# Kernel tuning notes

Measured on AMD Instinct MI355X. Metric: run time of the kernel, lower is better.

Reference implementation:

```python
import itertools
import jax, jax.numpy as jnp
import numpy as np

# static block configuration
B, C, H, W, DIM, HEADS = 2, 4, 60, 120, 512, 8
WS = (2, 6, 12)          # window size (Wc, Wh, Ww)
SS = (1, 3, 6)           # shift size
N = WS[0] * WS[1] * WS[2]            # 144 tokens per window
C1, H1, W1 = C // WS[0], H // WS[1], W // WS[2]
NW = C1 * H1 * W1                    # windows per sample
DH = DIM // HEADS
EPS = 1e-6


def _attn_bias():
    """Static shifted-window attention bias (nW, N, N): 0 within group, -inf across.
    Mirrors compute_3d_shifted_window_mask (warped=True, longitude wrap merge)."""
    img = np.zeros((C, H, W), np.int32)
    c_sl = ((0, C - WS[0]), (C - WS[0], C - SS[0]), (C - SS[0], C))
    h_sl = ((0, H - WS[1]), (H - WS[1], H - SS[1]), (H - SS[1], H))
    w_sl = ((0, W - WS[2]), (W - WS[2], W - SS[2]), (W - SS[2], W))
    cnt = 0
    for (cs, ce), (hs, he), (ws_, we) in itertools.product(c_sl, h_sl, w_sl):
        img[cs:ce, hs:he, ws_:we] = cnt
        cnt += 1
    # warped (periodic longitude) group merges
    for i in range(3):
        for a, b in ((1, 2), (4, 5), (7, 8)):
            img[img == a + 9 * i] = b + 9 * i
    m = img.reshape(C1, WS[0], H1, WS[1], W1, WS[2])
    m = m.transpose(0, 2, 4, 1, 3, 5).reshape(NW, N)
    diff = m[:, None, :] - m[:, :, None]
    return jnp.asarray(np.where(diff != 0, -np.inf, 0.0).astype(np.float32))


_BIAS = _attn_bias()[None, :, None, :, :]  # (1, nW, 1, N, N)


def _ln(x, s, b):
    mu = x.mean(-1, keepdims=True)
    var = x.var(-1, keepdims=True)
    return (x - mu) / jnp.sqrt(var + EPS) * s + b


def setup_inputs() -> dict:
    key = jax.random.key(0)
    ks = jax.random.split(key, 6)
    s = 0.02
    return {
        "x": jax.random.normal(ks[0], (B, C * H * W, DIM), jnp.float32),
        "qkv_w": jax.random.normal(ks[1], (DIM, 3 * DIM), jnp.float32) * s,
        "qkv_b": jnp.zeros((3 * DIM,), jnp.float32),
        "proj_w": jax.random.normal(ks[2], (DIM, DIM), jnp.float32) * s,
        "proj_b": jnp.zeros((DIM,), jnp.float32),
        "norm1_scale": jnp.ones((DIM,), jnp.float32),
        "norm1_bias": jnp.zeros((DIM,), jnp.float32),
        "norm2_scale": jnp.ones((DIM,), jnp.float32),
        "norm2_bias": jnp.zeros((DIM,), jnp.float32),
        "mlp_w1": jax.random.normal(ks[3], (DIM, 4 * DIM), jnp.float32) * s,
        "mlp_b1": jnp.zeros((4 * DIM,), jnp.float32),
        "mlp_w2": jax.random.normal(ks[4], (4 * DIM, DIM), jnp.float32) * s,
        "mlp_b2": jnp.zeros((DIM,), jnp.float32),
    }


def reference(x, qkv_w, qkv_b, proj_w, proj_b, norm1_scale, norm1_bias,
              norm2_scale, norm2_bias, mlp_w1, mlp_b1, mlp_w2, mlp_b2):
    shortcut = x                                   # (B, L, D)
    h = _ln(x, norm1_scale, norm1_bias).reshape(B, C, H, W, DIM)
    # cyclic shift
    h = jnp.roll(h, (-SS[0], -SS[1], -SS[2]), axis=(1, 2, 3))
    # window partition: (B,C,H,W,D) -> (B*nW, N, D)
    h = h.reshape(B, C1, WS[0], H1, WS[1], W1, WS[2], DIM)
    h = h.transpose(0, 1, 3, 5, 2, 4, 6, 7).reshape(B * NW, N, DIM)
    # windowed multi-head self-attention
    qkv = h @ qkv_w + qkv_b                        # (B*nW, N, 3*D)
    qkv = qkv.reshape(B, NW, N, 3, HEADS, DH)
    q = qkv[..., 0, :, :].transpose(0, 1, 3, 2, 4)  # (B, nW, H, N, Dh)
    k = qkv[..., 1, :, :].transpose(0, 1, 3, 2, 4)
    v = qkv[..., 2, :, :].transpose(0, 1, 3, 2, 4)
    scale = 1.0 / float(np.sqrt(DH))
    attn = jnp.einsum("bwhnd,bwhmd->bwhnm", q, k) * scale + _BIAS
    attn = jax.nn.softmax(attn, axis=-1)
    o = jnp.einsum("bwhnm,bwhmd->bwhnd", attn, v)
    o = o.transpose(0, 1, 3, 2, 4).reshape(B * NW, N, DIM)
    o = o @ proj_w + proj_b
    # window reverse: (B*nW, N, D) -> (B,C,H,W,D)
    o = o.reshape(B, C1, H1, W1, WS[0], WS[1], WS[2], DIM)
    o = o.transpose(0, 1, 4, 2, 5, 3, 6, 7).reshape(B, C, H, W, DIM)
    # reverse cyclic shift
    o = jnp.roll(o, SS, axis=(1, 2, 3))
    x = shortcut + o.reshape(B, C * H * W, DIM)    # drop_path is identity
    # MLP block
    h2 = _ln(x, norm2_scale, norm2_bias)
    h2 = jax.nn.gelu(h2 @ mlp_w1 + mlp_b1) @ mlp_w2 + mlp_b2
    return x + h2
```

## Files before the change

kernel.cpp:

```cpp
#include <hip/hip_runtime.h>

typedef __attribute__((ext_vector_type(8))) short bf16x8;
typedef __attribute__((ext_vector_type(4))) float f32x4;
typedef __attribute__((ext_vector_type(8))) unsigned short u16x8;

#define BAR() __builtin_amdgcn_s_barrier()
#define VMC(n) asm volatile("s_waitcnt vmcnt(" #n ")" ::: "memory")
#define SB0() __builtin_amdgcn_sched_barrier(0)
#define WAITL(n) do { asm volatile("s_waitcnt lgkmcnt(" #n ")"); SB0(); } while (0)
#define DSRI(dst, base, imm) \
  asm volatile("ds_read_b128 %0, %1 offset:%2" : "=&v"(dst) : "v"(base), "i"(imm))

__device__ inline unsigned short f2bf(float f) {
  unsigned int u = __float_as_uint(f);
  u += 0x7fffu + ((u >> 16) & 1u);
  return (unsigned short)(u >> 16);
}

__device__ inline void gload_lds16(const void* g, void* l) {
  __builtin_amdgcn_global_load_lds(
      (const __attribute__((address_space(1))) void*)g,
      (__attribute__((address_space(3))) void*)l, 16, 0, 0);
}

__global__ void wtrans(const float* __restrict__ W, unsigned short* __restrict__ Wt,
                       int K, int N) {
  int idx = blockIdx.x * 256 + threadIdx.x;
  if (idx >= K * N) return;
  int k = idx / N, n = idx - k * N;
  Wt[(size_t)n * K + k] = f2bf(W[idx]);
}

template <int MODE>
__global__ void ln_k(const float* __restrict__ x, const float* __restrict__ sc,
                     const float* __restrict__ bi, unsigned short* __restrict__ o) {
  int t = blockIdx.x * 4 + (threadIdx.x >> 6);
  int l = threadIdx.x & 63;
  size_t src;
  if (MODE == 0) {
    int b = t / 28800, r = t - b * 28800;
    int win = r / 144, tok = r - win * 144;
    int c1 = win / 100, rem = win - c1 * 100;
    int h1 = rem / 10, w1 = rem - h1 * 10;
    int tc = tok / 72, tr = tok - tc * 72;
    int th = tr / 12, tw = tr - th * 12;
    int cs = c1 * 2 + tc, hs = h1 * 6 + th, wsp = w1 * 12 + tw;
    int co = (cs + 1) & 3;
    int ho = hs + 3; if (ho >= 60) ho -= 60;
    int wo = wsp + 6; if (wo >= 120) wo -= 120;
    src = ((size_t)b * 28800 + (co * 60 + ho) * 120 + wo) * 512;
  } else {
    src = (size_t)t * 512;
  }
  const float4* xr = (const float4*)(x + src);
  float4 v0 = xr[l * 2], v1 = xr[l * 2 + 1];
  float s = v0.x + v0.y + v0.z + v0.w + v1.x + v1.y + v1.z + v1.w;
  float s2 = v0.x * v0.x + v0.y * v0.y + v0.z * v0.z + v0.w * v0.w +
             v1.x * v1.x + v1.y * v1.y + v1.z * v1.z + v1.w * v1.w;
  #pragma unroll
  for (int o2 = 32; o2; o2 >>= 1) {
    s += __shfl_xor(s, o2);
    s2 += __shfl_xor(s2, o2);
  }
  float mean = s * (1.0f / 512.0f);
  float var = s2 * (1.0f / 512.0f) - mean * mean;
  float inv = rsqrtf(var + 1e-6f);
  const float4* scp = (const float4*)sc;
  const float4* bip = (const float4*)bi;
  float4 sa = scp[l * 2], sb = scp[l * 2 + 1];
  float4 ba = bip[l * 2], bb = bip[l * 2 + 1];
  u16x8 ov;
  ov[0] = f2bf((v0.x - mean) * inv * sa.x + ba.x);
  ov[1] = f2bf((v0.y - mean) * inv * sa.y + ba.y);
  ov[2] = f2bf((v0.z - mean) * inv * sa.z + ba.z);
  ov[3] = f2bf((v0.w - mean) * inv * sa.w + ba.w);
  ov[4] = f2bf((v1.x - mean) * inv * sb.x + bb.x);
  ov[5] = f2bf((v1.y - mean) * inv * sb.y + bb.y);
  ov[6] = f2bf((v1.z - mean) * inv * sb.z + bb.z);
  ov[7] = f2bf((v1.w - mean) * inv * sb.w + bb.w);
  *(u16x8*)&o[(size_t)t * 512 + l * 8] = ov;
}

template <int EPI>
__launch_bounds__(512, 2)
__global__ void gemm2p(const unsigned short* __restrict__ A,
                       const unsigned short* __restrict__ Bt,
                       const float* __restrict__ bias, void* __restrict__ outp,
                       const float* __restrict__ res, int M, int N, int K) {
  __shared__ __attribute__((aligned(16))) unsigned short ldsb[2][32768];
  const int tid = threadIdx.x;
  const int w = tid >> 6, l = tid & 63;
  const int wm = w >> 2, wn = w & 3;
  const int lane15 = l & 15;
  const int ntile = N >> 8;
  const int nwg = gridDim.x;
  const int q = nwg >> 3, r = nwg & 7;
  const int xcd = blockIdx.x & 7, idx8 = blockIdx.x >> 3;
  const int wgid = (xcd < r ? xcd * (q + 1) : r * (q + 1) + (xcd - r) * q) + idx8;
  const int bm = wgid / ntile, bn = wgid - bm * ntile;
  const int NT = K >> 6;

  int offA[4];
  {
    int rowt = tid >> 3, slot = tid & 7;
    int sl = slot ^ (rowt & 7);
    #pragma unroll
    for (int jj = 0; jj < 4; ++jj)
      offA[jj] = ((jj * 64 + rowt) * K + sl * 8) * 2;
  }
  const char* gA = (const char*)(A + (size_t)bm * 256 * K);
  const char* gB = (const char*)(Bt + (size_t)bn * 256 * K);

  unsigned lds0 = (unsigned)(unsigned long long)
      (__attribute__((address_space(3))) void*)(void*)&ldsb[0][0];
  const int rsw = (((l >> 4) ^ (lane15 & 7)) << 4);
  unsigned rA0 = lds0 + (unsigned)((wm * 128 + lane15) * 128 + rsw);
  unsigned rB0 = lds0 + 32768u + (unsigned)((wn * 64 + lane15) * 128 + rsw);
  unsigned rA1 = rA0 + 65536u, rB1 = rB0 + 65536u;
  unsigned short* pC = &ldsb[0][0];
  unsigned short* pN = &ldsb[1][0];

  f32x4 acc[8][4] = {};
  bf16x8 af[8], bf[4], ag[8], bg[4];

  auto STAGE = [&](unsigned short* pS) {
    #pragma unroll
    for (int jj = 0; jj < 4; ++jj)
      gload_lds16(gA + offA[jj], pS + jj * 4096 + tid * 8);
    #pragma unroll
    for (int jj = 0; jj < 4; ++jj)
      gload_lds16(gB + offA[jj], pS + 16384 + jj * 4096 + tid * 8);
    gA += 128;
    gB += 128;
  };

  STAGE(pC);
  VMC(0);
  BAR();

  for (int t = 0; t < NT; ++t) {
    if (t < NT - 1) STAGE(pN);
    DSRI(af[0], rA0, 0);    DSRI(af[1], rA0, 2048);
    DSRI(af[2], rA0, 4096); DSRI(af[3], rA0, 6144);
    DSRI(af[4], rA0, 8192); DSRI(af[5], rA0, 10240);
    DSRI(af[6], rA0, 12288); DSRI(af[7], rA0, 14336);
    DSRI(bf[0], rB0, 0);    DSRI(bf[1], rB0, 2048);
    DSRI(bf[2], rB0, 4096); DSRI(bf[3], rB0, 6144);
    {
      unsigned rAx = rA0 ^ 64u, rBx = rB0 ^ 64u;
      DSRI(ag[0], rAx, 0);    DSRI(ag[1], rAx, 2048);
      DSRI(ag[2], rAx, 4096); DSRI(ag[3], rAx, 6144);
      DSRI(ag[4], rAx, 8192); DSRI(ag[5], rAx, 10240);
      DSRI(ag[6], rAx, 12288); DSRI(ag[7], rAx, 14336);
      DSRI(bg[0], rBx, 0);    DSRI(bg[1], rBx, 2048);
      DSRI(bg[2], rBx, 4096); DSRI(bg[3], rBx, 6144);
    }
    WAITL(12);
    __builtin_amdgcn_s_setprio(1);
    #pragma unroll
    for (int mi = 0; mi < 8; ++mi)
      #pragma unroll
      for (int nf = 0; nf < 4; ++nf)
        acc[mi][nf] = __builtin_amdgcn_mfma_f32_16x16x32_bf16(
            af[mi], bf[nf], acc[mi][nf], 0, 0, 0);
    __builtin_amdgcn_s_setprio(0);
    WAITL(0);
    __builtin_amdgcn_s_setprio(1);
    #pragma unroll
    for (int mi = 0; mi < 8; ++mi)
      #pragma unroll
      for (int nf = 0; nf < 4; ++nf)
        acc[mi][nf] = __builtin_amdgcn_mfma_f32_16x16x32_bf16(
            ag[mi], bg[nf], acc[mi][nf], 0, 0, 0);
    __builtin_amdgcn_s_setprio(0);
    VMC(0);
    BAR();
    { unsigned tt = rA0; rA0 = rA1; rA1 = tt; }
    { unsigned tt = rB0; rB0 = rB1; rB1 = tt; }
    { unsigned short* tp = pC; pC = pN; pN = tp; }
  }

  float* outf = (float*)outp;
  unsigned short* outh = (unsigned short*)outp;
  #pragma unroll
  for (int mi = 0; mi < 8; ++mi) {
    #pragma unroll
    for (int j = 0; j < 4; ++j) {
      int grow = bm * 256 + wm * 128 + mi * 16 + ((l >> 4) << 2) + j;
      int win = 0, tok = 0;
      size_t rowbase = 0;
      if constexpr (EPI == 0) {
        win = grow / 144;
        tok = grow - win * 144;
      } else if constexpr (EPI == 1) {
        win = grow / 144;
        tok = grow - win * 144;
        int b = win / 200, wl = win - b * 200;
        int c1 = wl / 100, rem = wl - c1 * 100;
        int h1 = rem / 10, w1 = rem - h1 * 10;
        int tc = tok / 72, tr = tok - tc * 72;
        int th = tr / 12, tw = tr - th * 12;
        int cs = c1 * 2 + tc, hs = h1 * 6 + th, wsp = w1 * 12 + tw;
        int co = (cs + 1) & 3;
        int ho = hs + 3; if (ho >= 60) ho -= 60;
        int wo = wsp + 6; if (wo >= 120) wo -= 120;
        rowbase = ((size_t)b * 28800 + (co * 60 + ho) * 120 + wo) * 512;
      }
      #pragma unroll
      for (int nf = 0; nf < 4; ++nf) {
        int gcol = bn * 256 + wn * 64 + nf * 16 + lane15;
        float val = acc[mi][nf][j] + bias[gcol];
        if constexpr (EPI == 0) {
          int which = gcol >> 9, hd = (gcol >> 6) & 7, dh = gcol & 63;
          outh[(((size_t)(win * 3 + which) * 8 + hd) * 144 + tok) * 64 + dh] = f2bf(val);
        } else if constexpr (EPI == 1) {
          size_t oi = rowbase + gcol;
          outf[oi] = res[oi] + val;
        } else if constexpr (EPI == 2) {
          float u = 0.7978845608f * (val + 0.044715f * val * val * val);
          float g = val / (1.0f + __expf(-2.0f * u));
          outh[(size_t)grow * N + gcol] = f2bf(g);
        } else {
          size_t oi = (size_t)grow * N + gcol;
          outf[oi] += val;
        }
      }
    }
  }
}

__launch_bounds__(576)
__global__ void attn_k(const unsigned short* __restrict__ qkv,
                       unsigned short* __restrict__ owin) {
  __shared__ __attribute__((aligned(16))) unsigned short Ks[144 * 72];
  __shared__ __attribute__((aligned(16))) unsigned short Vt[64 * 168];
  __shared__ __attribute__((aligned(16))) unsigned short Ps[144 * 168];
  __shared__ unsigned char gid[144];
  int bid = blockIdx.x;
  int win = bid >> 3, head = bid & 7;
  const unsigned short* qb = qkv + ((size_t)(win * 3 + 0) * 8 + head) * (144 * 64);
  const unsigned short* kb = qkv + ((size_t)(win * 3 + 1) * 8 + head) * (144 * 64);
  const unsigned short* vb = qkv + ((size_t)(win * 3 + 2) * 8 + head) * (144 * 64);
  int tid = threadIdx.x;
  {
    int row = tid >> 2, c0 = (tid & 3) << 4;
    u16x8 ka = *(const u16x8*)(kb + row * 64 + c0);
    u16x8 kc = *(const u16x8*)(kb + row * 64 + c0 + 8);
    *(u16x8*)&Ks[row * 72 + c0] = ka;
    *(u16x8*)&Ks[row * 72 + c0 + 8] = kc;
    u16x8 va = *(const u16x8*)(vb + row * 64 + c0);
    u16x8 vc = *(const u16x8*)(vb + row * 64 + c0 + 8);
    #pragma unroll
    for (int j = 0; j < 8; ++j) Vt[(c0 + j) * 168 + row] = va[j];
    #pragma unroll
    for (int j = 0; j < 8; ++j) Vt[(c0 + 8 + j) * 168 + row] = vc[j];
  }
  for (int i = tid; i < 64 * 24; i += 576) {
    int d = i / 24, m = i - d * 24;
    Vt[d * 168 + 144 + m] = 0;
  }
  for (int i = tid; i < 144 * 24; i += 576) {
    int r = i / 24, c = i - r * 24;
    Ps[r * 168 + 144 + c] = 0;
  }
  if (tid < 144) {
    int wl = win % 200;
    int c1 = wl / 100, rem = wl - c1 * 100;
    int h1 = rem / 10, w1 = rem - h1 * 10;
    int tc = tid / 72, tr = tid - tc * 72;
    int th = tr / 12, tw = tr - th * 12;
    int cs = c1 * 2 + tc, hs = h1 * 6 + th, wsp = w1 * 12 + tw;
    int rc = cs < 2 ? 0 : (cs < 3 ? 1 : 2);
    int rh = hs < 54 ? 0 : (hs < 57 ? 1 : 2);
    int rw = wsp < 108 ? 0 : (wsp < 114 ? 1 : 2);
    if (rw == 1) rw = 2;
    gid[tid] = (unsigned char)(rc * 9 + rh * 3 + rw);
  }
  __syncthreads();
  int wv = tid >> 6, l = tid & 63;
  int lane15 = l & 15, lk = (l >> 4) << 3;
  bf16x8 aq0 = *(const bf16x8*)(qb + (wv * 16 + lane15) * 64 + lk);
  bf16x8 aq1 = *(const bf16x8*)(qb + (wv * 16 + lane15) * 64 + 32 + lk);
  f32x4 sf[9];
  #pragma unroll
  for (int ct = 0; ct < 9; ++ct) {
    f32x4 z = {};
    bf16x8 b0 = *(const bf16x8*)&Ks[(ct * 16 + lane15) * 72 + lk];
    bf16x8 b1 = *(const bf16x8*)&Ks[(ct * 16 + lane15) * 72 + 32 + lk];
    z = __builtin_amdgcn_mfma_f32_16x16x32_bf16(aq0, b0, z, 0, 0, 0);
    z = __builtin_amdgcn_mfma_f32_16x16x32_bf16(aq1, b1, z, 0, 0, 0);
    sf[ct] = z;
  }
  int gi[4];
  #pragma unroll
  for (int j = 0; j < 4; ++j) gi[j] = gid[wv * 16 + ((l >> 4) << 2) + j];
  float mx[4] = {-1e30f, -1e30f, -1e30f, -1e30f};
  #pragma unroll
  for (int ct = 0; ct < 9; ++ct) {
    int gj = gid[ct * 16 + lane15];
    #pragma unroll
    for (int j = 0; j < 4; ++j) {
      float s = sf[ct][j] * 0.125f;
      if (gj != gi[j]) s = -1e30f;
      sf[ct][j] = s;
      mx[j] = fmaxf(mx[j], s);
    }
  }
  #pragma unroll
  for (int o2 = 8; o2; o2 >>= 1)
    #pragma unroll
    for (int j = 0; j < 4; ++j) mx[j] = fmaxf(mx[j], __shfl_xor(mx[j], o2));
  float sm[4] = {0.f, 0.f, 0.f, 0.f};
  #pragma unroll
  for (int ct = 0; ct < 9; ++ct)
    #pragma unroll
    for (int j = 0; j < 4; ++j) {
      float e = __expf(sf[ct][j] - mx[j]);
      sf[ct][j] = e;
      sm[j] += e;
    }
  #pragma unroll
  for (int o2 = 8; o2; o2 >>= 1)
    #pragma unroll
    for (int j = 0; j < 4; ++j) sm[j] += __shfl_xor(sm[j], o2);
  float rs[4];
  #pragma unroll
  for (int j = 0; j < 4; ++j) rs[j] = 1.0f / sm[j];
  #pragma unroll
  for (int ct = 0; ct < 9; ++ct)
    #pragma unroll
    for (int j = 0; j < 4; ++j)
      Ps[(wv * 16 + ((l >> 4) << 2) + j) * 168 + ct * 16 + lane15] =
          f2bf(sf[ct][j] * rs[j]);
  __syncthreads();
  f32x4 of[4] = {};
  #pragma unroll
  for (int ks = 0; ks < 5; ++ks) {
    bf16x8 ap = *(const bf16x8*)&Ps[(wv * 16 + lane15) * 168 + ks * 32 + lk];
    #pragma unroll
    for (int nt = 0; nt < 4; ++nt) {
      bf16x8 bv = *(const bf16x8*)&Vt[(nt * 16 + lane15) * 168 + ks * 32 + lk];
      of[nt] = __builtin_amdgcn_mfma_f32_16x16x32_bf16(ap, bv, of[nt], 0, 0, 0);
    }
  }
  unsigned short* ob = owin + (size_t)win * 144 * 512 + head * 64;
  #pragma unroll
  for (int nt = 0; nt < 4; ++nt)
    #pragma unroll
    for (int j = 0; j < 4; ++j) {
      int row = wv * 16 + ((l >> 4) << 2) + j;
      ob[(size_t)row * 512 + nt * 16 + lane15] = f2bf(of[nt][j]);
    }
}

extern "C" void kernel_launch(void* const* d_in, const int* in_sizes, int n_in,
                              void* d_out, int out_size, void* d_ws, size_t ws_size,
                              hipStream_t stream) {
  const float* x = (const float*)d_in[0];
  const float* qkv_w = (const float*)d_in[1];
  const float* qkv_b = (const float*)d_in[2];
  const float* proj_w = (const float*)d_in[3];
  const float* proj_b = (const float*)d_in[4];
  const float* n1s = (const float*)d_in[5];
  const float* n1b = (const float*)d_in[6];
  const float* n2s = (const float*)d_in[7];
  const float* n2b = (const float*)d_in[8];
  const float* w1 = (const float*)d_in[9];
  const float* b1 = (const float*)d_in[10];
  const float* w2 = (const float*)d_in[11];
  const float* b2 = (const float*)d_in[12];
  float* out = (float*)d_out;
  char* ws = (char*)d_ws;

  unsigned short* WqT = (unsigned short*)(ws);
  unsigned short* WpT = (unsigned short*)(ws + 1572864);
  unsigned short* W1T = (unsigned short*)(ws + 2097152);
  unsigned short* W2T = (unsigned short*)(ws + 4194304);
  unsigned short* hwin = (unsigned short*)(ws + 6291456);
  unsigned short* qkvb = (unsigned short*)(ws + 65273856);
  unsigned short* owin = (unsigned short*)(ws + 242221056);
  unsigned short* mid = qkvb;

  wtrans<<<(512 * 1536 + 255) / 256, 256, 0, stream>>>(qkv_w, WqT, 512, 1536);
  wtrans<<<(512 * 512 + 255) / 256, 256, 0, stream>>>(proj_w, WpT, 512, 512);
  wtrans<<<(512 * 2048 + 255) / 256, 256, 0, stream>>>(w1, W1T, 512, 2048);
  wtrans<<<(2048 * 512 + 255) / 256, 256, 0, stream>>>(w2, W2T, 2048, 512);
  ln_k<0><<<14400, 256, 0, stream>>>(x, n1s, n1b, hwin);
  gemm2p<0><<<225 * 6, 512, 0, stream>>>(hwin, WqT, qkv_b, qkvb, nullptr, 57600, 1536, 512);
  attn_k<<<3200, 576, 0, stream>>>(qkvb, owin);
  gemm2p<1><<<225 * 2, 512, 0, stream>>>(owin, WpT, proj_b, out, x, 57600, 512, 512);
  ln_k<1><<<14400, 256, 0, stream>>>(out, n2s, n2b, hwin);
  gemm2p<2><<<225 * 8, 512, 0, stream>>>(hwin, W1T, b1, mid, nullptr, 57600, 2048, 512);
  gemm2p<3><<<225 * 2, 512, 0, stream>>>(mid, W2T, b2, out, nullptr, 57600, 512, 2048);
}
```

Before: 790.7 us.

## Restructure GEMM into 4-buffer K=32 pipeline with split A/B staging

Replaces the double-buffered K=64 GEMM main loop with a four-slot ring of K=32 tiles prefetched two steps ahead. A and B loads are issued separately, interleaved with two half-M MFMA phases separated by barriers. This keeps more global loads in flight and cuts register pressure by halving the fragment registers. The cost is more barriers per unit of K and a new LDS swizzle for 64-byte rows, which could cause bank conflicts or more sync stalls.

```diff
diff --git a/kernel.cpp b/kernel.cpp
--- a/kernel.cpp
+++ b/kernel.cpp
@@ -7,7 +7,7 @@
 #define BAR() __builtin_amdgcn_s_barrier()
 #define VMC(n) asm volatile("s_waitcnt vmcnt(" #n ")" ::: "memory")
 #define SB0() __builtin_amdgcn_sched_barrier(0)
-#define WAITL(n) do { asm volatile("s_waitcnt lgkmcnt(" #n ")"); SB0(); } while (0)
+#define WAITL0() do { asm volatile("s_waitcnt lgkmcnt(0)"); SB0(); } while (0)
 #define DSRI(dst, base, imm) \
   asm volatile("ds_read_b128 %0, %1 offset:%2" : "=&v"(dst) : "v"(base), "i"(imm))
 
@@ -83,11 +83,11 @@
 
 template <int EPI>
 __launch_bounds__(512, 2)
-__global__ void gemm2p(const unsigned short* __restrict__ A,
+__global__ void gemm8p(const unsigned short* __restrict__ A,
                        const unsigned short* __restrict__ Bt,
                        const float* __restrict__ bias, void* __restrict__ outp,
                        const float* __restrict__ res, int M, int N, int K) {
-  __shared__ __attribute__((aligned(16))) unsigned short ldsb[2][32768];
+  __shared__ __attribute__((aligned(16))) unsigned short lds8[4][16384];
   const int tid = threadIdx.x;
   const int w = tid >> 6, l = tid & 63;
   const int wm = w >> 2, wn = w & 3;
@@ -98,86 +98,80 @@
   const int xcd = blockIdx.x & 7, idx8 = blockIdx.x >> 3;
   const int wgid = (xcd < r ? xcd * (q + 1) : r * (q + 1) + (xcd - r) * q) + idx8;
   const int bm = wgid / ntile, bn = wgid - bm * ntile;
-  const int NT = K >> 6;
-
-  int offA[4];
-  {
-    int rowt = tid >> 3, slot = tid & 7;
-    int sl = slot ^ (rowt & 7);
-    #pragma unroll
-    for (int jj = 0; jj < 4; ++jj)
-      offA[jj] = ((jj * 64 + rowt) * K + sl * 8) * 2;
-  }
+  const int KT = K >> 5;
+  const int Kb = K * 2;
+
+  const int srow = tid >> 2;
+  const int ssl = (tid & 3) ^ ((srow >> 1) & 3);
+  const int offAB = srow * Kb + ssl * 16;
+  char* const ldsc = (char*)&lds8[0][0];
+
   const char* gA = (const char*)(A + (size_t)bm * 256 * K);
   const char* gB = (const char*)(Bt + (size_t)bn * 256 * K);
 
   unsigned lds0 = (unsigned)(unsigned long long)
-      (__attribute__((address_space(3))) void*)(void*)&ldsb[0][0];
-  const int rsw = (((l >> 4) ^ (lane15 & 7)) << 4);
-  unsigned rA0 = lds0 + (unsigned)((wm * 128 + lane15) * 128 + rsw);
-  unsigned rB0 = lds0 + 32768u + (unsigned)((wn * 64 + lane15) * 128 + rsw);
-  unsigned rA1 = rA0 + 65536u, rB1 = rB0 + 65536u;
-  unsigned short* pC = &ldsb[0][0];
-  unsigned short* pN = &ldsb[1][0];
+      (__attribute__((address_space(3))) void*)(void*)&lds8[0][0];
+  const unsigned swz = (unsigned)((((l >> 4) ^ ((lane15 >> 1) & 3)) << 4));
+  const unsigned rA0 = lds0 + (unsigned)((wm * 128 + lane15) * 64) + swz;
+  const unsigned rB0 = lds0 + 16384u + (unsigned)((wn * 64 + lane15) * 64) + swz;
 
   f32x4 acc[8][4] = {};
-  bf16x8 af[8], bf[4], ag[8], bg[4];
-
-  auto STAGE = [&](unsigned short* pS) {
-    #pragma unroll
-    for (int jj = 0; jj < 4; ++jj)
-      gload_lds16(gA + offA[jj], pS + jj * 4096 + tid * 8);
-    #pragma unroll
-    for (int jj = 0; jj < 4; ++jj)
-      gload_lds16(gB + offA[jj], pS + 16384 + jj * 4096 + tid * 8);
-    gA += 128;
-    gB += 128;
+  bf16x8 af[4], bf[4];
+
+  auto STAGE_A = [&](int bufi, const char* gat) {
+    char* dst = ldsc + bufi * 32768 + w * 1024;
+    gload_lds16(gat + offAB, dst);
+    gload_lds16(gat + offAB + 128 * Kb, dst + 8192);
   };
-
-  STAGE(pC);
-  VMC(0);
+  auto STAGE_B = [&](int bufi, const char* gbt) {
+    char* dst = ldsc + bufi * 32768 + 16384 + w * 1024;
+    gload_lds16(gbt + offAB, dst);
+    gload_lds16(gbt + offAB + 128 * Kb, dst + 8192);
+  };
+
+  STAGE_A(0, gA); STAGE_B(0, gB);
+  STAGE_A(1, gA + 64); STAGE_B(1, gB + 64);
+  VMC(4);
   BAR();
 
-  for (int t = 0; t < NT; ++t) {
-    if (t < NT - 1) STAGE(pN);
-    DSRI(af[0], rA0, 0);    DSRI(af[1], rA0, 2048);
-    DSRI(af[2], rA0, 4096); DSRI(af[3], rA0, 6144);
-    DSRI(af[4], rA0, 8192); DSRI(af[5], rA0, 10240);
-    DSRI(af[6], rA0, 12288); DSRI(af[7], rA0, 14336);
-    DSRI(bf[0], rB0, 0);    DSRI(bf[1], rB0, 2048);
-    DSRI(bf[2], rB0, 4096); DSRI(bf[3], rB0, 6144);
-    {
-      unsigned rAx = rA0 ^ 64u, rBx = rB0 ^ 64u;
-      DSRI(ag[0], rAx, 0);    DSRI(ag[1], rAx, 2048);
-      DSRI(ag[2], rAx, 4096); DSRI(ag[3], rAx, 6144);
-      DSRI(ag[4], rAx, 8192); DSRI(ag[5], rAx, 10240);
-      DSRI(ag[6], rAx, 12288); DSRI(ag[7], rAx, 14336);
-      DSRI(bg[0], rBx, 0);    DSRI(bg[1], rBx, 2048);
-      DSRI(bg[2], rBx, 4096); DSRI(bg[3], rBx, 6144);
-    }
-    WAITL(12);
+  for (int t = 0; t < KT; ++t) {
+    const unsigned boff = (unsigned)((t & 3) << 15);
+    const unsigned rAb = rA0 + boff, rBb = rB0 + boff;
+    const bool st = (t + 2 < KT);
+    const int bufS = (t + 2) & 3;
+    const char* gAt = gA + (size_t)(t + 2) * 64;
+    const char* gBt = gB + (size_t)(t + 2) * 64;
+    DSRI(af[0], rAb, 0);    DSRI(af[1], rAb, 1024);
+    DSRI(af[2], rAb, 2048); DSRI(af[3], rAb, 3072);
+    DSRI(bf[0], rBb, 0);    DSRI(bf[1], rBb, 1024);
+    DSRI(bf[2], rBb, 2048); DSRI(bf[3], rBb, 3072);
+    if (st) STAGE_A(bufS, gAt);
+    BAR();
+    WAITL0();
     __builtin_amdgcn_s_setprio(1);
     #pragma unroll
-    for (int mi = 0; mi < 8; ++mi)
+    for (int mi = 0; mi < 4; ++mi)
       #pragma unroll
       for (int nf = 0; nf < 4; ++nf)
         acc[mi][nf] = __builtin_amdgcn_mfma_f32_16x16x32_bf16(
             af[mi], bf[nf], acc[mi][nf], 0, 0, 0);
     __builtin_amdgcn_s_setprio(0);
-    WAITL(0);
+    BAR();
+    DSRI(af[0], rAb, 4096); DSRI(af[1], rAb, 5120);
+    DSRI(af[2], rAb, 6144); DSRI(af[3], rAb, 7168);
+    if (st) STAGE_B(bufS, gBt);
+    if (t < KT - 2) { VMC(4); } else if (t == KT - 2) { VMC(0); }
+    BAR();
+    WAITL0();
     __builtin_amdgcn_s_setprio(1);
     #pragma unroll
-    for (int mi = 0; mi < 8; ++mi)
+    for (int mi = 0; mi < 4; ++mi)
       #pragma unroll
       for (int nf = 0; nf < 4; ++nf)
-        acc[mi][nf] = __builtin_amdgcn_mfma_f32_16x16x32_bf16(
-            ag[mi], bg[nf], acc[mi][nf], 0, 0, 0);
+        acc[4 + mi][nf] = __builtin_amdgcn_mfma_f32_16x16x32_bf16(
+            af[mi], bf[nf], acc[4 + mi][nf], 0, 0, 0);
     __builtin_amdgcn_s_setprio(0);
-    VMC(0);
     BAR();
-    { unsigned tt = rA0; rA0 = rA1; rA1 = tt; }
-    { unsigned tt = rB0; rB0 = rB1; rB1 = tt; }
-    { unsigned short* tp = pC; pC = pN; pN = tp; }
   }
 
   float* outf = (float*)outp;
@@ -386,10 +380,10 @@
   wtrans<<<(512 * 2048 + 255) / 256, 256, 0, stream>>>(w1, W1T, 512, 2048);
   wtrans<<<(2048 * 512 + 255) / 256, 256, 0, stream>>>(w2, W2T, 2048, 512);
   ln_k<0><<<14400, 256, 0, stream>>>(x, n1s, n1b, hwin);
-  gemm2p<0><<<225 * 6, 512, 0, stream>>>(hwin, WqT, qkv_b, qkvb, nullptr, 57600, 1536, 512);
+  gemm8p<0><<<225 * 6, 512, 0, stream>>>(hwin, WqT, qkv_b, qkvb, nullptr, 57600, 1536, 512);
   attn_k<<<3200, 576, 0, stream>>>(qkvb, owin);
-  gemm2p<1><<<225 * 2, 512, 0, stream>>>(owin, WpT, proj_b, out, x, 57600, 512, 512);
+  gemm8p<1><<<225 * 2, 512, 0, stream>>>(owin, WpT, proj_b, out, x, 57600, 512, 512);
   ln_k<1><<<14400, 256, 0, stream>>>(out, n2s, n2b, hwin);
-  gemm2p<2><<<225 * 8, 512, 0, stream>>>(hwin, W1T, b1, mid, nullptr, 57600, 2048, 512);
-  gemm2p<3><<<225 * 2, 512, 0, stream>>>(mid, W2T, b2, out, nullptr, 57600, 512, 2048);
-}
+  gemm8p<2><<<225 * 8, 512, 0, stream>>>(hwin, W1T, b1, mid, nullptr, 57600, 2048, 512);
+  gemm8p<3><<<225 * 2, 512, 0, stream>>>(mid, W2T, b2, out, nullptr, 57600, 512, 2048);
+}
```

After: 810.3 us. +2.5%, slower.
